# Kernel tuning notes

Hardware: AMD Instinct MI355X
Metric: run time of the kernel (lower is better)

## Reference

```python
import jax, jax.numpy as jnp
import numpy as np

B, N, D_IN, D_OUT = 8, 2048, 256, 256
BN_EPS = 1e-5
SELU_ALPHA = 1.6732632423543772
SELU_SCALE = 1.0507009873554805


def setup_inputs() -> dict:
    key = jax.random.key(0)
    k1, k2, k3, k4 = jax.random.split(key, 4)
    lim_lin = 1.0 / np.sqrt(D_IN)
    return {
        "x": jax.random.normal(k1, (B, N, D_IN), dtype=jnp.float32),
        "w_map": jax.random.uniform(k2, (D_IN,), jnp.float32, -lim_lin, lim_lin),
        "w_att": jax.random.uniform(k3, (D_OUT, D_IN), jnp.float32, -lim_lin, lim_lin),
        "w_res": jax.random.uniform(k4, (D_OUT, D_IN), jnp.float32, -lim_lin, lim_lin),
        "gamma": jnp.ones((D_OUT,), jnp.float32),
        "beta": jnp.zeros((D_OUT,), jnp.float32),
    }


def _selu(x):
    x_clamped = jnp.clip(x, -10.0, 10.0)
    return SELU_SCALE * jnp.where(x > 0, x, SELU_ALPHA * (jnp.exp(x_clamped) - 1.0))


def reference(x, w_map, w_att, w_res, gamma, beta):
    # scores[b,i,j] = sum_d w_map[d] * x[b,i,d] * x[b,j,d]  (== W_map(x_i*x_j))
    scores = jnp.einsum("bid,bjd->bij", x * w_map, x)  # [B,N,N]
    attn = jax.nn.softmax(scores, axis=-1)
    aggregated = jnp.einsum("bij,bjd->bid", attn, x)  # [B,N,D]
    out = aggregated @ w_att.T + x @ w_res.T  # [B,N,D_OUT]
    # BatchNorm1d in training mode: stats over (batch, nodes) per channel, biased var
    mean = jnp.mean(out, axis=(0, 1))
    var = jnp.mean(jnp.square(out - mean), axis=(0, 1))
    out = (out - mean) * jax.lax.rsqrt(var + BN_EPS) * gamma + beta
    return _selu(out)
```

## Files before the change

kernel.cpp:

```cpp
#include <hip/hip_runtime.h>
#include <hip/hip_bf16.h>


typedef __attribute__((ext_vector_type(8)))  short bf16x8;
typedef __attribute__((ext_vector_type(4)))  float f32x4;
typedef __attribute__((ext_vector_type(16))) float f32x16;

#define MFMA16(a, b, c) __builtin_amdgcn_mfma_f32_16x16x32_bf16((a), (b), (c), 0, 0, 0)
#define MFMA32(a, b, c) __builtin_amdgcn_mfma_f32_32x32x16_bf16((a), (b), (c), 0, 0, 0)

constexpr int   NB = 8, NN = 2048;
constexpr int   ROWS = NB * NN;
constexpr float BN_EPS = 1e-5f;
constexpr float SELU_ALPHA = 1.6732632423543772f;
constexpr float SELU_SCALE = 1.0507009873554805f;

__device__ __forceinline__ unsigned short f2bf(float f) {
  union { float f; unsigned int u; } v; v.f = f;
  unsigned int u = v.u;
  u += 0x7FFFu + ((u >> 16) & 1u);
  return (unsigned short)(u >> 16);
}
__device__ __forceinline__ float bf2f(unsigned short h) {
  union { float f; unsigned int u; } v; v.u = ((unsigned int)h) << 16;
  return v.f;
}

__device__ __forceinline__ void async_copy16(const unsigned short* g, unsigned short* l) {
  __builtin_amdgcn_global_load_lds(
      (const __attribute__((address_space(1))) void*)g,
      (__attribute__((address_space(3))) void*)l, 16, 0, 0);
}

__global__ __launch_bounds__(256) void k0_prep(const float* __restrict__ x,
                                               unsigned short* __restrict__ XR,
                                               unsigned short* __restrict__ Xt,
                                               const float* __restrict__ w_att,
                                               const float* __restrict__ w_res,
                                               unsigned short* __restrict__ WC,
                                               float* __restrict__ sums) {
  __shared__ unsigned short Ls[64 * 264];
  const int t = threadIdx.x;
  const int b = blockIdx.x & 7, rt = blockIdx.x >> 3;
  const int grb = b * NN + rt * 64;
  const int c = (t & 31) * 8, r0 = t >> 5;
#pragma unroll
  for (int q = 0; q < 8; ++q) {
    int r = r0 + q * 8;
    const float* xp = x + (size_t)(grb + r) * 256 + c;
    float4 a = *(const float4*)xp;
    float4 d = *(const float4*)(xp + 4);
    union { unsigned short s[8]; uint4 v; } xb;
    xb.s[0] = f2bf(a.x); xb.s[1] = f2bf(a.y); xb.s[2] = f2bf(a.z); xb.s[3] = f2bf(a.w);
    xb.s[4] = f2bf(d.x); xb.s[5] = f2bf(d.y); xb.s[6] = f2bf(d.z); xb.s[7] = f2bf(d.w);
    *(uint4*)(XR + (size_t)(grb + r) * 256 + c) = xb.v;
    *(uint4*)&Ls[r * 264 + c] = xb.v;
  }
  __syncthreads();
  unsigned short* dst = Xt + ((size_t)b * 256 + t) * 2048 + rt * 64;
#pragma unroll
  for (int k = 0; k < 8; ++k) {
    union { unsigned short s[8]; uint4 v; } o;
#pragma unroll
    for (int j = 0; j < 8; ++j) o.s[j] = Ls[(k * 8 + j) * 264 + t];
    *(uint4*)(dst + k * 8) = o.v;
  }
  if (blockIdx.x == 0 && t < 256) ((float4*)sums)[t] = make_float4(0.f, 0.f, 0.f, 0.f);
  if (blockIdx.x < 64) {
    int f = (blockIdx.x * 256 + t) * 8;
    int cc = f >> 9, k = f & 511;
    const float* src = (k < 256) ? (w_att + cc * 256 + k) : (w_res + cc * 256 + (k - 256));
    float4 a = *(const float4*)src;
    float4 d = *(const float4*)(src + 4);
    union { unsigned short s[8]; uint4 v; } o;
    o.s[0] = f2bf(a.x); o.s[1] = f2bf(a.y); o.s[2] = f2bf(a.z); o.s[3] = f2bf(a.w);
    o.s[4] = f2bf(d.x); o.s[5] = f2bf(d.y); o.s[6] = f2bf(d.z); o.s[7] = f2bf(d.w);
    *(uint4*)(WC + f) = o.v;
  }
}

__global__ __launch_bounds__(512, 2) void k1_attn(const float* __restrict__ w_map,
                                                  const unsigned short* __restrict__ XR,
                                                  const unsigned short* __restrict__ Xt,
                                                  unsigned short* __restrict__ Opart,
                                                  float* __restrict__ Lpart) {
  __shared__ unsigned short Ks[2][32 * 256];
  __shared__ unsigned short Vt[2][256 * 32];
  __shared__ unsigned short Psw[8][32 * 40];

  const int t = threadIdx.x;
  const int w = t >> 6, lane = t & 63;
  const int l15 = lane & 15, quad = lane >> 4;
  const int l31 = lane & 31, h = lane >> 5;
  const int qb = blockIdx.x >> 2, p = blockIdx.x & 3;
  const int b = qb >> 3;
  const int rowbase = qb * 256;
  const int jb0 = b * 2048 + p * 512;
  const unsigned short* Xtb = Xt + (size_t)b * 256 * 2048;

  int kSrc[2], vSrc[2];
#pragma unroll
  for (int q = 0; q < 2; ++q) {
    int cch = q * 512 + t;
    int kj = cch >> 5, kck = cch & 31;
    kSrc[q] = (jb0 + kj) * 256 + ((kck ^ (kj & 7)) * 8);
    int vd = cch >> 2, vcj = cch & 3;
    vSrc[q] = vd * 2048 + p * 512 + ((vcj ^ ((vd >> 1) & 3)) * 8);
  }

  bf16x8 qf[2][8];
#pragma unroll
  for (int qn = 0; qn < 2; ++qn) {
    const unsigned short* xrow = XR + (size_t)(rowbase + w * 32 + qn * 16 + l15) * 256;
#pragma unroll
    for (int kc = 0; kc < 8; ++kc) {
      bf16x8 xb = *(const bf16x8*)(xrow + kc * 32 + quad * 8);
      const float* wp = w_map + kc * 32 + quad * 8;
      float4 w0 = *(const float4*)wp, w1 = *(const float4*)(wp + 4);
      float wv[8] = {w0.x, w0.y, w0.z, w0.w, w1.x, w1.y, w1.z, w1.w};
      bf16x8 q;
#pragma unroll
      for (int i = 0; i < 8; ++i)
        q[i] = (short)f2bf(bf2f((unsigned short)xb[i]) * wv[i]);
      qf[qn][kc] = q;
    }
  }

  const f32x16 fz16 = {0.f,0.f,0.f,0.f, 0.f,0.f,0.f,0.f, 0.f,0.f,0.f,0.f, 0.f,0.f,0.f,0.f};
  f32x16 oacc[8];
#pragma unroll
  for (int i = 0; i < 8; ++i) oacc[i] = fz16;
  float rsum0 = 0.f, rsum1 = 0.f;

  const int sw7 = l15 & 7;
  const int vkey = (l31 >> 1) & 3;

#pragma unroll
  for (int q = 0; q < 2; ++q)
    async_copy16(XR + kSrc[q], &Ks[0][(q * 512 + t) * 8]);
#pragma unroll
  for (int q = 0; q < 2; ++q)
    async_copy16(Xtb + vSrc[q], &Vt[0][(q * 512 + t) * 8]);

  for (int jt = 0; jt < 16; ++jt) {
    const int cur = jt & 1;
    __syncthreads();
    if (jt < 15) {
#pragma unroll
      for (int q = 0; q < 2; ++q)
        async_copy16(XR + kSrc[q] + (jt + 1) * 8192, &Ks[cur ^ 1][(q * 512 + t) * 8]);
#pragma unroll
      for (int q = 0; q < 2; ++q)
        async_copy16(Xtb + vSrc[q] + (jt + 1) * 32, &Vt[cur ^ 1][(q * 512 + t) * 8]);
    }
    const f32x4 fz = {0.f, 0.f, 0.f, 0.f};
    f32x4 s00 = fz, s01 = fz, s10 = fz, s11 = fz;
#pragma unroll
    for (int kc = 0; kc < 8; ++kc) {
      const int ck = ((kc * 4 + quad) ^ sw7) * 8;
      bf16x8 kf0 = *(const bf16x8*)&Ks[cur][l15 * 256 + ck];
      bf16x8 kf1 = *(const bf16x8*)&Ks[cur][(16 + l15) * 256 + ck];
      s00 = MFMA16(kf0, qf[0][kc], s00);
      s01 = MFMA16(kf0, qf[1][kc], s01);
      s10 = MFMA16(kf1, qf[0][kc], s10);
      s11 = MFMA16(kf1, qf[1][kc], s11);
    }
#pragma unroll
    for (int qn = 0; qn < 2; ++qn) {
#pragma unroll
      for (int jm = 0; jm < 2; ++jm) {
        f32x4 sv = (qn == 0) ? (jm == 0 ? s00 : s10) : (jm == 0 ? s01 : s11);
        float e0 = __expf(sv[0]), e1 = __expf(sv[1]);
        float e2 = __expf(sv[2]), e3 = __expf(sv[3]);
        if (qn == 0) rsum0 += (e0 + e1) + (e2 + e3);
        else         rsum1 += (e0 + e1) + (e2 + e3);
        ushort4 pk;
        pk.x = f2bf(e0); pk.y = f2bf(e1); pk.z = f2bf(e2); pk.w = f2bf(e3);
        *(ushort4*)&Psw[w][(qn * 16 + l15) * 40 + jm * 16 + quad * 4] = pk;
      }
    }
    bf16x8 af0 = *(const bf16x8*)&Psw[w][l31 * 40 + h * 8];
    bf16x8 af1 = *(const bf16x8*)&Psw[w][l31 * 40 + 16 + h * 8];
#pragma unroll
    for (int dt = 0; dt < 8; ++dt) {
      const int dbase = (dt * 32 + l31) * 32;
      bf16x8 v0 = *(const bf16x8*)&Vt[cur][dbase + ((h ^ vkey) * 8)];
      oacc[dt] = MFMA32(af0, v0, oacc[dt]);
      bf16x8 v1 = *(const bf16x8*)&Vt[cur][dbase + (((2 + h) ^ vkey) * 8)];
      oacc[dt] = MFMA32(af1, v1, oacc[dt]);
    }
  }

#pragma unroll
  for (int qn = 0; qn < 2; ++qn) {
    float rs = (qn == 0) ? rsum0 : rsum1;
    rs += __shfl_xor(rs, 16);
    rs += __shfl_xor(rs, 32);
    if (quad == 0) Lpart[(size_t)p * ROWS + rowbase + w * 32 + qn * 16 + l15] = rs;
  }
  unsigned short* ob = Opart + (size_t)p * ROWS * 256 + (size_t)(rowbase + w * 32) * 256 + l31;
#pragma unroll
  for (int dt = 0; dt < 8; ++dt)
#pragma unroll
    for (int r = 0; r < 16; ++r) {
      int qrow = (r & 3) + ((r >> 2) << 3) + (h << 2);
      ob[qrow * 256 + dt * 32] = f2bf(oacc[dt][r]);
    }
}

__global__ __launch_bounds__(256, 2) void k2_gemm(const unsigned short* __restrict__ XR,
                                                  const unsigned short* __restrict__ Opart,
                                                  const float* __restrict__ Lpart,
                                                  const unsigned short* __restrict__ WC,
                                                  float* __restrict__ out,
                                                  float* __restrict__ sums) {
  __shared__ unsigned short As[128 * 72];
  __shared__ unsigned short Bs[64 * 72];
  __shared__ float cs[64], cq[64];
  __shared__ float invLs[128];
  const int t = threadIdx.x;
  const int w = t >> 6, lane = t & 63, l15 = lane & 15, quad = lane >> 4;
  const int m0 = (blockIdx.x >> 2) * 128, n0 = (blockIdx.x & 3) * 64;
  if (t < 128) {
    int row = m0 + t;
    invLs[t] = 1.0f / (Lpart[row] + Lpart[ROWS + row] +
                       Lpart[2 * ROWS + row] + Lpart[3 * ROWS + row]);
  }
  if (t < 64) { cs[t] = 0.f; cq[t] = 0.f; }

  const f32x4 fz = {0.f, 0.f, 0.f, 0.f};
  f32x4 acc[4][2];
#pragma unroll
  for (int i = 0; i < 4; ++i) { acc[i][0] = fz; acc[i][1] = fz; }

  for (int kk = 0; kk < 512; kk += 64) {
    __syncthreads();
    if (kk < 256) {
#pragma unroll
      for (int q = 0; q < 4; ++q) {
        int idx = t + q * 256;
        int row = idx >> 3, koff = (idx & 7) * 8;
        size_t base = (size_t)(m0 + row) * 256 + kk + koff;
        union { unsigned short s[8]; uint4 v; } p0, p1, p2, p3;
        p0.v = *(const uint4*)(Opart + base);
        p1.v = *(const uint4*)(Opart + (size_t)ROWS * 256 + base);
        p2.v = *(const uint4*)(Opart + (size_t)2 * ROWS * 256 + base);
        p3.v = *(const uint4*)(Opart + (size_t)3 * ROWS * 256 + base);
        float il = invLs[row];
        union { unsigned short s[8]; uint4 v; } o;
#pragma unroll
        for (int e = 0; e < 8; ++e) {
          float f = (bf2f(p0.s[e]) + bf2f(p1.s[e])) + (bf2f(p2.s[e]) + bf2f(p3.s[e]));
          o.s[e] = f2bf(f * il);
        }
        *(uint4*)&As[row * 72 + koff] = o.v;
      }
    } else {
#pragma unroll
      for (int q = 0; q < 4; ++q) {
        int idx = t + q * 256;
        int row = idx >> 3, koff = (idx & 7) * 8;
        *(uint4*)&As[row * 72 + koff] =
            *(const uint4*)(XR + (size_t)(m0 + row) * 256 + (kk - 256) + koff);
      }
    }
#pragma unroll
    for (int q = 0; q < 2; ++q) {
      int idx = t + q * 256;
      int row = idx >> 3, koff = (idx & 7) * 8;
      *(uint4*)&Bs[row * 72 + koff] = *(const uint4*)(WC + (size_t)(n0 + row) * 512 + kk + koff);
    }
    __syncthreads();
#pragma unroll
    for (int kc = 0; kc < 2; ++kc) {
      bf16x8 b0 = *(const bf16x8*)&Bs[((w >> 1) * 32 + l15) * 72 + kc * 32 + quad * 8];
      bf16x8 b1 = *(const bf16x8*)&Bs[((w >> 1) * 32 + 16 + l15) * 72 + kc * 32 + quad * 8];
#pragma unroll
      for (int mt = 0; mt < 4; ++mt) {
        bf16x8 af = *(const bf16x8*)&As[((w & 1) * 64 + mt * 16 + l15) * 72 + kc * 32 + quad * 8];
        acc[mt][0] = MFMA16(af, b0, acc[mt][0]);
        acc[mt][1] = MFMA16(af, b1, acc[mt][1]);
      }
    }
  }
#pragma unroll
  for (int mt = 0; mt < 4; ++mt)
#pragma unroll
    for (int nt = 0; nt < 2; ++nt)
#pragma unroll
      for (int r = 0; r < 4; ++r) {
        int grow = m0 + (w & 1) * 64 + mt * 16 + quad * 4 + r;
        int gcol = n0 + (w >> 1) * 32 + nt * 16 + l15;
        out[(size_t)grow * 256 + gcol] = acc[mt][nt][r];
      }
#pragma unroll
  for (int nt = 0; nt < 2; ++nt) {
    float a = 0.f, b2 = 0.f;
#pragma unroll
    for (int mt = 0; mt < 4; ++mt)
#pragma unroll
      for (int r = 0; r < 4; ++r) {
        float v = acc[mt][nt][r];
        a += v; b2 += v * v;
      }
    a += __shfl_xor(a, 16);  a += __shfl_xor(a, 32);
    b2 += __shfl_xor(b2, 16); b2 += __shfl_xor(b2, 32);
    if (quad == 0) {
      int ci = (w >> 1) * 32 + nt * 16 + l15;
      atomicAdd(&cs[ci], a);
      atomicAdd(&cq[ci], b2);
    }
  }
  __syncthreads();
  if (t < 64) {
    atomicAdd(&sums[n0 + t], cs[t]);
    atomicAdd(&sums[256 + n0 + t], cq[t]);
  }
}

__global__ __launch_bounds__(256) void k4_bn_selu(float* __restrict__ out,
                                                  const float* __restrict__ sums,
                                                  const float* __restrict__ gamma,
                                                  const float* __restrict__ beta) {
  int f = (blockIdx.x * 256 + threadIdx.x) * 8;
  int c = f & 255;
  const float inv_m = 1.0f / 16384.0f;
  float4 v0 = *(const float4*)(out + f);
  float4 v1 = *(const float4*)(out + f + 4);
  float vv[8] = {v0.x, v0.y, v0.z, v0.w, v1.x, v1.y, v1.z, v1.w};
#pragma unroll
  for (int k = 0; k < 8; ++k) {
    int ch = c + k;
    float mean = sums[ch] * inv_m;
    float var = sums[256 + ch] * inv_m - mean * mean;
    float y = (vv[k] - mean) * rsqrtf(var + BN_EPS) * gamma[ch] + beta[ch];
    float yc = fminf(fmaxf(y, -10.f), 10.f);
    float r = (y > 0.f) ? y : (SELU_ALPHA * (expf(yc) - 1.0f));
    vv[k] = SELU_SCALE * r;
  }
  float4 o0 = {vv[0], vv[1], vv[2], vv[3]};
  float4 o1 = {vv[4], vv[5], vv[6], vv[7]};
  *(float4*)(out + f) = o0;
  *(float4*)(out + f + 4) = o1;
}

extern "C" void kernel_launch(void* const* d_in, const int* in_sizes, int n_in,
                              void* d_out, int out_size, void* d_ws, size_t ws_size,
                              hipStream_t stream) {
  const float* x     = (const float*)d_in[0];
  const float* w_map = (const float*)d_in[1];
  const float* w_att = (const float*)d_in[2];
  const float* w_res = (const float*)d_in[3];
  const float* gamma = (const float*)d_in[4];
  const float* beta  = (const float*)d_in[5];
  float* out = (float*)d_out;

  unsigned short* XR = (unsigned short*)d_ws;
  unsigned short* Xt = XR + (size_t)ROWS * 256;
  unsigned short* WC = Xt + (size_t)NB * 256 * 2048;
  unsigned short* Opart = WC + 256 * 512;
  float* Lpart = (float*)(Opart + (size_t)4 * ROWS * 256);
  float* sums  = Lpart + 4 * ROWS;

  k0_prep<<<256, 256, 0, stream>>>(x, XR, Xt, w_att, w_res, WC, sums);
  k1_attn<<<256, 512, 0, stream>>>(w_map, XR, Xt, Opart, Lpart);
  k2_gemm<<<512, 256, 0, stream>>>(XR, Opart, Lpart, WC, out, sums);
  k4_bn_selu<<<2048, 256, 0, stream>>>(out, sums, gamma, beta);
}
```

Baseline: 164.0 us.

## Use 32x32 MFMA for scores with register-resident P and split combine kernel

The score GEMM in the attention kernel now uses 32x32x16 MFMA, and the K rows are permuted at load time so the score accumulator layout matches the A-operand layout of the PV MFMA. This lets P be packed directly from registers instead of going through an LDS round trip with per-wave buffers. The Q-fragment load is moved after the first async K/V prefetch. The partial-output combine and normalization moves out of the GEMM into a separate kernel writing into the reused Xt buffer, which simplifies the GEMM's A-tile load at the cost of an extra launch and an extra pass over memory.

```diff
diff --git a/kernel.cpp b/kernel.cpp
--- a/kernel.cpp
+++ b/kernel.cpp
@@ -24,6 +24,9 @@
 __device__ __forceinline__ float bf2f(unsigned short h) {
   union { float f; unsigned int u; } v; v.u = ((unsigned int)h) << 16;
   return v.f;
+}
+__device__ __forceinline__ unsigned int pk2(float lo, float hi) {
+  return (unsigned int)f2bf(lo) | ((unsigned int)f2bf(hi) << 16);
 }
 
 __device__ __forceinline__ void async_copy16(const unsigned short* g, unsigned short* l) {
@@ -86,11 +89,9 @@
                                                   float* __restrict__ Lpart) {
   __shared__ unsigned short Ks[2][32 * 256];
   __shared__ unsigned short Vt[2][256 * 32];
-  __shared__ unsigned short Psw[8][32 * 40];
 
   const int t = threadIdx.x;
   const int w = t >> 6, lane = t & 63;
-  const int l15 = lane & 15, quad = lane >> 4;
   const int l31 = lane & 31, h = lane >> 5;
   const int qb = blockIdx.x >> 2, p = blockIdx.x & 3;
   const int b = qb >> 3;
@@ -103,26 +104,33 @@
   for (int q = 0; q < 2; ++q) {
     int cch = q * 512 + t;
     int kj = cch >> 5, kck = cch & 31;
-    kSrc[q] = (jb0 + kj) * 256 + ((kck ^ (kj & 7)) * 8);
+    int pj = ((kj >> 3) & 1) * 16 + ((kj >> 4) & 1) * 4 + (kj & 3) + ((kj >> 2) & 1) * 8;
+    kSrc[q] = (jb0 + pj) * 256 + ((kck ^ (kj & 7)) * 8);
     int vd = cch >> 2, vcj = cch & 3;
     vSrc[q] = vd * 2048 + p * 512 + ((vcj ^ ((vd >> 1) & 3)) * 8);
   }
 
-  bf16x8 qf[2][8];
-#pragma unroll
-  for (int qn = 0; qn < 2; ++qn) {
-    const unsigned short* xrow = XR + (size_t)(rowbase + w * 32 + qn * 16 + l15) * 256;
-#pragma unroll
-    for (int kc = 0; kc < 8; ++kc) {
-      bf16x8 xb = *(const bf16x8*)(xrow + kc * 32 + quad * 8);
-      const float* wp = w_map + kc * 32 + quad * 8;
+#pragma unroll
+  for (int q = 0; q < 2; ++q)
+    async_copy16(XR + kSrc[q], &Ks[0][(q * 512 + t) * 8]);
+#pragma unroll
+  for (int q = 0; q < 2; ++q)
+    async_copy16(Xtb + vSrc[q], &Vt[0][(q * 512 + t) * 8]);
+
+  bf16x8 qf[16];
+  {
+    const unsigned short* xrow = XR + (size_t)(rowbase + w * 32 + l31) * 256 + h * 8;
+#pragma unroll
+    for (int kc = 0; kc < 16; ++kc) {
+      bf16x8 xb = *(const bf16x8*)(xrow + kc * 16);
+      const float* wp = w_map + kc * 16 + h * 8;
       float4 w0 = *(const float4*)wp, w1 = *(const float4*)(wp + 4);
       float wv[8] = {w0.x, w0.y, w0.z, w0.w, w1.x, w1.y, w1.z, w1.w};
-      bf16x8 q;
+      bf16x8 qv;
 #pragma unroll
       for (int i = 0; i < 8; ++i)
-        q[i] = (short)f2bf(bf2f((unsigned short)xb[i]) * wv[i]);
-      qf[qn][kc] = q;
+        qv[i] = (short)f2bf(bf2f((unsigned short)xb[i]) * wv[i]);
+      qf[kc] = qv;
     }
   }
 
@@ -130,17 +138,10 @@
   f32x16 oacc[8];
 #pragma unroll
   for (int i = 0; i < 8; ++i) oacc[i] = fz16;
-  float rsum0 = 0.f, rsum1 = 0.f;
-
-  const int sw7 = l15 & 7;
+  float rsum = 0.f;
+
+  const int sw7 = l31 & 7;
   const int vkey = (l31 >> 1) & 3;
-
-#pragma unroll
-  for (int q = 0; q < 2; ++q)
-    async_copy16(XR + kSrc[q], &Ks[0][(q * 512 + t) * 8]);
-#pragma unroll
-  for (int q = 0; q < 2; ++q)
-    async_copy16(Xtb + vSrc[q], &Vt[0][(q * 512 + t) * 8]);
 
   for (int jt = 0; jt < 16; ++jt) {
     const int cur = jt & 1;
@@ -153,52 +154,45 @@
       for (int q = 0; q < 2; ++q)
         async_copy16(Xtb + vSrc[q] + (jt + 1) * 32, &Vt[cur ^ 1][(q * 512 + t) * 8]);
     }
-    const f32x4 fz = {0.f, 0.f, 0.f, 0.f};
-    f32x4 s00 = fz, s01 = fz, s10 = fz, s11 = fz;
+    f32x16 sA = fz16, sB = fz16;
 #pragma unroll
     for (int kc = 0; kc < 8; ++kc) {
-      const int ck = ((kc * 4 + quad) ^ sw7) * 8;
-      bf16x8 kf0 = *(const bf16x8*)&Ks[cur][l15 * 256 + ck];
-      bf16x8 kf1 = *(const bf16x8*)&Ks[cur][(16 + l15) * 256 + ck];
-      s00 = MFMA16(kf0, qf[0][kc], s00);
-      s01 = MFMA16(kf0, qf[1][kc], s01);
-      s10 = MFMA16(kf1, qf[0][kc], s10);
-      s11 = MFMA16(kf1, qf[1][kc], s11);
-    }
-#pragma unroll
-    for (int qn = 0; qn < 2; ++qn) {
-#pragma unroll
-      for (int jm = 0; jm < 2; ++jm) {
-        f32x4 sv = (qn == 0) ? (jm == 0 ? s00 : s10) : (jm == 0 ? s01 : s11);
-        float e0 = __expf(sv[0]), e1 = __expf(sv[1]);
-        float e2 = __expf(sv[2]), e3 = __expf(sv[3]);
-        if (qn == 0) rsum0 += (e0 + e1) + (e2 + e3);
-        else         rsum1 += (e0 + e1) + (e2 + e3);
-        ushort4 pk;
-        pk.x = f2bf(e0); pk.y = f2bf(e1); pk.z = f2bf(e2); pk.w = f2bf(e3);
-        *(ushort4*)&Psw[w][(qn * 16 + l15) * 40 + jm * 16 + quad * 4] = pk;
-      }
-    }
-    bf16x8 af0 = *(const bf16x8*)&Psw[w][l31 * 40 + h * 8];
-    bf16x8 af1 = *(const bf16x8*)&Psw[w][l31 * 40 + 16 + h * 8];
+      bf16x8 kf = *(const bf16x8*)&Ks[cur][l31 * 256 + (((2 * kc + h) ^ sw7) * 8)];
+      sA = MFMA32(kf, qf[kc], sA);
+    }
+#pragma unroll
+    for (int kc = 8; kc < 16; ++kc) {
+      bf16x8 kf = *(const bf16x8*)&Ks[cur][l31 * 256 + (((2 * kc + h) ^ sw7) * 8)];
+      sB = MFMA32(kf, qf[kc], sB);
+    }
+    float pv[16];
+#pragma unroll
+    for (int r = 0; r < 16; ++r) {
+      pv[r] = __expf(sA[r] + sB[r]);
+      rsum += pv[r];
+    }
+    union { unsigned int u[4]; bf16x8 v; } a0, a1;
+    a0.u[0] = pk2(pv[0],  pv[1]);
+    a0.u[1] = pk2(pv[2],  pv[3]);
+    a0.u[2] = pk2(pv[8],  pv[9]);
+    a0.u[3] = pk2(pv[10], pv[11]);
+    a1.u[0] = pk2(pv[4],  pv[5]);
+    a1.u[1] = pk2(pv[6],  pv[7]);
+    a1.u[2] = pk2(pv[12], pv[13]);
+    a1.u[3] = pk2(pv[14], pv[15]);
 #pragma unroll
     for (int dt = 0; dt < 8; ++dt) {
       const int dbase = (dt * 32 + l31) * 32;
       bf16x8 v0 = *(const bf16x8*)&Vt[cur][dbase + ((h ^ vkey) * 8)];
-      oacc[dt] = MFMA32(af0, v0, oacc[dt]);
+      oacc[dt] = MFMA32(a0.v, v0, oacc[dt]);
       bf16x8 v1 = *(const bf16x8*)&Vt[cur][dbase + (((2 + h) ^ vkey) * 8)];
-      oacc[dt] = MFMA32(af1, v1, oacc[dt]);
-    }
-  }
-
-#pragma unroll
-  for (int qn = 0; qn < 2; ++qn) {
-    float rs = (qn == 0) ? rsum0 : rsum1;
-    rs += __shfl_xor(rs, 16);
-    rs += __shfl_xor(rs, 32);
-    if (quad == 0) Lpart[(size_t)p * ROWS + rowbase + w * 32 + qn * 16 + l15] = rs;
-  }
-  unsigned short* ob = Opart + (size_t)p * ROWS * 256 + (size_t)(rowbase + w * 32) * 256 + l31;
+      oacc[dt] = MFMA32(a1.v, v1, oacc[dt]);
+    }
+  }
+
+  float rsT = rsum + __shfl_xor(rsum, 32);
+  if (h == 0) Lpart[(size_t)p * ROWS + rowbase + w * 32 + l31] = rsT;
+  unsigned short* ob = Opart + ((size_t)p * ROWS + rowbase + w * 32) * 256 + l31;
 #pragma unroll
   for (int dt = 0; dt < 8; ++dt)
 #pragma unroll
@@ -208,24 +202,37 @@
     }
 }
 
+__global__ __launch_bounds__(256) void kc_comb(const unsigned short* __restrict__ Opart,
+                                               const float* __restrict__ Lpart,
+                                               unsigned short* __restrict__ Oagg) {
+  const int t = threadIdx.x;
+  const int row = blockIdx.x * 8 + (t >> 5);
+  const int col = (t & 31) * 8;
+  const float invL = 1.0f / (Lpart[row] + Lpart[ROWS + row] +
+                             Lpart[2 * ROWS + row] + Lpart[3 * ROWS + row]);
+  const size_t base = (size_t)row * 256 + col;
+  union { unsigned short s[8]; uint4 v; } p0, p1, p2, p3, o;
+  p0.v = *(const uint4*)(Opart + base);
+  p1.v = *(const uint4*)(Opart + (size_t)ROWS * 256 + base);
+  p2.v = *(const uint4*)(Opart + (size_t)2 * ROWS * 256 + base);
+  p3.v = *(const uint4*)(Opart + (size_t)3 * ROWS * 256 + base);
+#pragma unroll
+  for (int e = 0; e < 8; ++e)
+    o.s[e] = f2bf(((bf2f(p0.s[e]) + bf2f(p1.s[e])) + (bf2f(p2.s[e]) + bf2f(p3.s[e]))) * invL);
+  *(uint4*)(Oagg + base) = o.v;
+}
+
 __global__ __launch_bounds__(256, 2) void k2_gemm(const unsigned short* __restrict__ XR,
-                                                  const unsigned short* __restrict__ Opart,
-                                                  const float* __restrict__ Lpart,
+                                                  const unsigned short* __restrict__ Oagg,
                                                   const unsigned short* __restrict__ WC,
                                                   float* __restrict__ out,
                                                   float* __restrict__ sums) {
   __shared__ unsigned short As[128 * 72];
   __shared__ unsigned short Bs[64 * 72];
   __shared__ float cs[64], cq[64];
-  __shared__ float invLs[128];
   const int t = threadIdx.x;
   const int w = t >> 6, lane = t & 63, l15 = lane & 15, quad = lane >> 4;
   const int m0 = (blockIdx.x >> 2) * 128, n0 = (blockIdx.x & 3) * 64;
-  if (t < 128) {
-    int row = m0 + t;
-    invLs[t] = 1.0f / (Lpart[row] + Lpart[ROWS + row] +
-                       Lpart[2 * ROWS + row] + Lpart[3 * ROWS + row]);
-  }
   if (t < 64) { cs[t] = 0.f; cq[t] = 0.f; }
 
   const f32x4 fz = {0.f, 0.f, 0.f, 0.f};
@@ -235,34 +242,14 @@
 
   for (int kk = 0; kk < 512; kk += 64) {
     __syncthreads();
-    if (kk < 256) {
-#pragma unroll
-      for (int q = 0; q < 4; ++q) {
-        int idx = t + q * 256;
-        int row = idx >> 3, koff = (idx & 7) * 8;
-        size_t base = (size_t)(m0 + row) * 256 + kk + koff;
-        union { unsigned short s[8]; uint4 v; } p0, p1, p2, p3;
-        p0.v = *(const uint4*)(Opart + base);
-        p1.v = *(const uint4*)(Opart + (size_t)ROWS * 256 + base);
-        p2.v = *(const uint4*)(Opart + (size_t)2 * ROWS * 256 + base);
-        p3.v = *(const uint4*)(Opart + (size_t)3 * ROWS * 256 + base);
-        float il = invLs[row];
-        union { unsigned short s[8]; uint4 v; } o;
-#pragma unroll
-        for (int e = 0; e < 8; ++e) {
-          float f = (bf2f(p0.s[e]) + bf2f(p1.s[e])) + (bf2f(p2.s[e]) + bf2f(p3.s[e]));
-          o.s[e] = f2bf(f * il);
-        }
-        *(uint4*)&As[row * 72 + koff] = o.v;
-      }
-    } else {
-#pragma unroll
-      for (int q = 0; q < 4; ++q) {
-        int idx = t + q * 256;
-        int row = idx >> 3, koff = (idx & 7) * 8;
-        *(uint4*)&As[row * 72 + koff] =
-            *(const uint4*)(XR + (size_t)(m0 + row) * 256 + (kk - 256) + koff);
-      }
+#pragma unroll
+    for (int q = 0; q < 4; ++q) {
+      int idx = t + q * 256;
+      int row = idx >> 3, koff = (idx & 7) * 8;
+      const unsigned short* src = (kk < 256)
+          ? (Oagg + (size_t)(m0 + row) * 256 + kk + koff)
+          : (XR + (size_t)(m0 + row) * 256 + (kk - 256) + koff);
+      *(uint4*)&As[row * 72 + koff] = *(const uint4*)src;
     }
 #pragma unroll
     for (int q = 0; q < 2; ++q) {
@@ -361,9 +348,11 @@
   unsigned short* Opart = WC + 256 * 512;
   float* Lpart = (float*)(Opart + (size_t)4 * ROWS * 256);
   float* sums  = Lpart + 4 * ROWS;
+  unsigned short* Oagg = Xt;
 
   k0_prep<<<256, 256, 0, stream>>>(x, XR, Xt, w_att, w_res, WC, sums);
   k1_attn<<<256, 512, 0, stream>>>(w_map, XR, Xt, Opart, Lpart);
-  k2_gemm<<<512, 256, 0, stream>>>(XR, Opart, Lpart, WC, out, sums);
+  kc_comb<<<2048, 256, 0, stream>>>(Opart, Lpart, Oagg);
+  k2_gemm<<<512, 256, 0, stream>>>(XR, Oagg, WC, out, sums);
   k4_bn_selu<<<2048, 256, 0, stream>>>(out, sums, gamma, beta);
 }
```

Measured after the change: 163.0 us. About the same (-0.6%).
